# Optimization experiments

Hardware: AMD Instinct MI355X
Metric: run time of the kernel (lower is better)

The kernel has to match this reference:

```python
import jax, jax.numpy as jnp
import numpy as np

EPS = 1e-12  # guard sqrt at zero


def setup_inputs() -> dict:
    key = jax.random.key(0)
    k1, k2, k3 = jax.random.split(key, 3)
    B, N = 16, 2048
    pred_points = jax.random.normal(k1, (B, N, 3), dtype=jnp.float32)
    target_points = jax.random.normal(k2, (B, N, 3), dtype=jnp.float32)
    # binary symmetry flag per object, kept float for the blend
    sym_flag = (jax.random.uniform(k3, (B,)) > 0.5).astype(jnp.float32)
    return {"pred_points": pred_points, "target_points": target_points, "sym_flag": sym_flag}


def reference(pred_points, target_points, sym_flag):
    # Chamfer (ADD-S style): per pred point, min Euclidean distance to any target point.
    # Pairwise squared distances via ||p||^2 + ||t||^2 - 2 p.t  -> [B, N, M]
    p2 = jnp.sum(pred_points * pred_points, axis=-1)[:, :, None]   # [B,N,1]
    t2 = jnp.sum(target_points * target_points, axis=-1)[:, None, :]  # [B,1,M]
    cross = jnp.einsum('bnd,bmd->bnm', pred_points, target_points)  # [B,N,M]
    d2 = p2 + t2 - 2.0 * cross
    dist = jnp.sqrt(jnp.maximum(d2, EPS))                           # [B,N,M]
    sym_dis = jnp.min(dist, axis=2).mean(axis=1)                    # [B]

    # L2 (ADD style): per-point correspondence distance.
    asym_dis = jnp.linalg.norm(pred_points - target_points, axis=2).mean(axis=1)  # [B]

    all_loss = sym_flag * sym_dis + (1.0 - sym_flag) * asym_dis
    return all_loss.mean()
```

## Files before the change

kernel.cpp:

```cpp
#include <hip/hip_runtime.h>
#include <hip/hip_bf16.h>
#include <math.h>


typedef short short8 __attribute__((ext_vector_type(8)));
typedef float f32x16 __attribute__((ext_vector_type(16)));

__device__ __forceinline__ unsigned short f2bf(float f) {
  unsigned u = __float_as_uint(f);
  u = u + 0x7FFFu + ((u >> 16) & 1u);
  return (unsigned short)(u >> 16);
}
__device__ __forceinline__ float bf2f(unsigned short h) {
  return __uint_as_float(((unsigned)h) << 16);
}

#define K1_TPB 256
#define TQS 512
#define PPANEL 256

__global__ __launch_bounds__(K1_TPB) void chamfer_mfma_kernel(
    const float* __restrict__ pred, const float* __restrict__ targ,
    float* __restrict__ minS, float* __restrict__ out, int N, int B) {
  __shared__ short8 sA[2][TQS];

  const int blk = blockIdx.x;
  const int tq = blk & 3;
  const int pp = (blk >> 2) & 7;
  const int b = blk >> 5;

  if (blk == 0 && threadIdx.x == 0) out[0] = 0.f;

  const float* tb = targ + ((size_t)b * N + tq * TQS) * 3;
  for (int t = threadIdx.x; t < TQS; t += K1_TPB) {
    const float x = tb[t * 3], y = tb[t * 3 + 1], z = tb[t * 3 + 2];
    const unsigned short thx = f2bf(x), thy = f2bf(y), thz = f2bf(z);
    const unsigned short tlx = f2bf(x - bf2f(thx));
    const unsigned short tly = f2bf(y - bf2f(thy));
    const unsigned short tlz = f2bf(z - bf2f(thz));
    const float q = 0.5f * (x * x + y * y + z * z);
    const unsigned short qh = f2bf(q), ql = f2bf(q - bf2f(qh));
    sA[0][t] = short8{(short)thx, (short)thy, (short)thz, (short)thx,
                      (short)thy, (short)thz, (short)tlx, (short)tly};
    sA[1][t] = short8{(short)tlz, (short)qh, (short)ql, 0, 0, 0, 0, 0};
  }

  const int lane = threadIdx.x & 63;
  const int w = threadIdx.x >> 6;
  const int g = lane >> 5;
  const int l31 = lane & 31;
  const int colBase = pp * PPANEL + w * 64;

  short8 bf0, bf1;
  {
#pragma unroll
    for (int pt = 0; pt < 2; ++pt) {
      const int c = colBase + pt * 32 + l31;
      const float* pq = pred + ((size_t)b * N + c) * 3;
      const float x = pq[0], y = pq[1], z = pq[2];
      const unsigned short hx = f2bf(-x), hy = f2bf(-y), hz = f2bf(-z);
      const unsigned short lx = f2bf(-x - bf2f(hx));
      const unsigned short ly = f2bf(-y - bf2f(hy));
      const unsigned short lz = f2bf(-z - bf2f(hz));
      short8 r;
      if (g == 0)
        r = short8{(short)hx, (short)hy, (short)hz, (short)lx,
                   (short)ly, (short)lz, (short)hx, (short)hy};
      else
        r = short8{(short)hz, (short)0x3F80, (short)0x3F80, 0, 0, 0, 0, 0};
      if (pt == 0) bf0 = r; else bf1 = r;
    }
  }
  __syncthreads();

  const f32x16 zc = {0.f, 0.f, 0.f, 0.f, 0.f, 0.f, 0.f, 0.f,
                     0.f, 0.f, 0.f, 0.f, 0.f, 0.f, 0.f, 0.f};
  float rm0[8], rm1[8];
#pragma unroll
  for (int i = 0; i < 8; ++i) { rm0[i] = 3.4e38f; rm1[i] = 3.4e38f; }

#pragma unroll 4
  for (int ta = 0; ta < TQS / 32; ++ta) {
    const short8 a = sA[g][ta * 32 + l31];
    const f32x16 d0 = __builtin_amdgcn_mfma_f32_32x32x16_bf16(a, bf0, zc, 0, 0, 0);
    const f32x16 d1 = __builtin_amdgcn_mfma_f32_32x32x16_bf16(a, bf1, zc, 0, 0, 0);
#pragma unroll
    for (int i = 0; i < 8; ++i) {
      rm0[i] = fminf(rm0[i], fminf(d0[2 * i], d0[2 * i + 1]));
      rm1[i] = fminf(rm1[i], fminf(d1[2 * i], d1[2 * i + 1]));
    }
  }

  float m0 = rm0[0], m1 = rm1[0];
#pragma unroll
  for (int i = 1; i < 8; ++i) { m0 = fminf(m0, rm0[i]); m1 = fminf(m1, rm1[i]); }
  m0 = fminf(m0, __shfl_xor(m0, 32));
  m1 = fminf(m1, __shfl_xor(m1, 32));

  if (lane < 32) {
    float* dst = minS + ((size_t)(b * 4 + tq)) * N;
    dst[colBase + lane] = m0;
    dst[colBase + 32 + lane] = m1;
  }
}

__global__ __launch_bounds__(256) void chamfer_final_kernel(
    const float* __restrict__ pred, const float* __restrict__ targ,
    const float* __restrict__ minS, const float* __restrict__ sym_flag,
    float* __restrict__ out, int N, int B, float invNB) {
  const int blk = blockIdx.x;
  const int b = blk >> 3;
  const int i = (blk & 7) * 256 + threadIdx.x;
  const size_t col = (size_t)b * N + i;

  float m = minS[(size_t)(b * 4 + 0) * N + i];
  m = fminf(m, minS[(size_t)(b * 4 + 1) * N + i]);
  m = fminf(m, minS[(size_t)(b * 4 + 2) * N + i]);
  m = fminf(m, minS[(size_t)(b * 4 + 3) * N + i]);

  const float px = pred[col * 3], py = pred[col * 3 + 1], pz = pred[col * 3 + 2];
  const float tx = targ[col * 3], ty = targ[col * 3 + 1], tz = targ[col * 3 + 2];
  const float hp2 = 0.5f * (px * px + py * py + pz * pz);
  const float dsym = sqrtf(fmaxf(2.f * (m + hp2), 1e-12f));
  const float dx = px - tx, dy = py - ty, dz = pz - tz;
  const float dasym = sqrtf(dx * dx + dy * dy + dz * dz);
  const float f = sym_flag[b];

  float c = (f * dsym + (1.f - f) * dasym) * invNB;
#pragma unroll
  for (int off = 32; off > 0; off >>= 1) c += __shfl_xor(c, off);
  __shared__ float sW[4];
  if ((threadIdx.x & 63) == 0) sW[threadIdx.x >> 6] = c;
  __syncthreads();
  if (threadIdx.x == 0) atomicAdd(out, sW[0] + sW[1] + sW[2] + sW[3]);
}

extern "C" void kernel_launch(void* const* d_in, const int* in_sizes, int n_in,
                              void* d_out, int out_size, void* d_ws, size_t ws_size,
                              hipStream_t stream) {
  const float* pred = (const float*)d_in[0];
  const float* targ = (const float*)d_in[1];
  const float* sym_flag = (const float*)d_in[2];
  float* out = (float*)d_out;

  const int B = in_sizes[2];
  const int N = in_sizes[0] / (B * 3);

  float* minS = (float*)d_ws;

  const int grid1 = B * 4 * (N / PPANEL);
  chamfer_mfma_kernel<<<grid1, K1_TPB, 0, stream>>>(pred, targ, minS, out, N, B);

  const int grid2 = B * (N / 256);
  chamfer_final_kernel<<<grid2, 256, 0, stream>>>(
      pred, targ, minS, sym_flag, out, N, B, 1.0f / (float)(N * B));
}
```

Baseline: 15.94 us.

## Fuse min-reduction and loss into MFMA kernel with full target set per block

Each block now loads the entire 2048-point target set for its batch into shared memory and processes 128 pred columns, so it computes the full nearest-neighbour minimum without splitting targets across blocks. The per-point sym/asym loss is then computed in the same kernel and written as per-wave partials. A single-block kernel sums them deterministically, replacing the global-memory min buffer, the second per-point pass and the atomic. The trade-off is that every block re-packs all 2048 targets into 64 KB of LDS, which cuts occupancy, and each wave issues one MFMA per step where it used to issue two.

```diff
diff --git a/kernel.cpp b/kernel.cpp
--- a/kernel.cpp
+++ b/kernel.cpp
@@ -15,24 +15,21 @@
   return __uint_as_float(((unsigned)h) << 16);
 }
 
-#define K1_TPB 256
-#define TQS 512
-#define PPANEL 256
+#define TPB 256
+#define NPTS 2048
 
-__global__ __launch_bounds__(K1_TPB) void chamfer_mfma_kernel(
+__global__ __launch_bounds__(TPB) void chamfer_fused_mfma_kernel(
     const float* __restrict__ pred, const float* __restrict__ targ,
-    float* __restrict__ minS, float* __restrict__ out, int N, int B) {
-  __shared__ short8 sA[2][TQS];
+    const float* __restrict__ sym_flag, float* __restrict__ partial,
+    int N, int B, int panelsPerBatch) {
+  __shared__ short8 sA[2][NPTS];
 
   const int blk = blockIdx.x;
-  const int tq = blk & 3;
-  const int pp = (blk >> 2) & 7;
-  const int b = blk >> 5;
+  const int pp = blk % panelsPerBatch;
+  const int b = blk / panelsPerBatch;
 
-  if (blk == 0 && threadIdx.x == 0) out[0] = 0.f;
-
-  const float* tb = targ + ((size_t)b * N + tq * TQS) * 3;
-  for (int t = threadIdx.x; t < TQS; t += K1_TPB) {
+  const float* tb = targ + (size_t)b * N * 3;
+  for (int t = threadIdx.x; t < N; t += TPB) {
     const float x = tb[t * 3], y = tb[t * 3 + 1], z = tb[t * 3 + 2];
     const unsigned short thx = f2bf(x), thy = f2bf(y), thz = f2bf(z);
     const unsigned short tlx = f2bf(x - bf2f(thx));
@@ -49,90 +46,68 @@
   const int w = threadIdx.x >> 6;
   const int g = lane >> 5;
   const int l31 = lane & 31;
-  const int colBase = pp * PPANEL + w * 64;
+  const int col = pp * 128 + w * 32 + l31;
 
-  short8 bf0, bf1;
+  const float* pq = pred + ((size_t)b * N + col) * 3;
+  const float px = pq[0], py = pq[1], pz = pq[2];
+  short8 bfr;
   {
-#pragma unroll
-    for (int pt = 0; pt < 2; ++pt) {
-      const int c = colBase + pt * 32 + l31;
-      const float* pq = pred + ((size_t)b * N + c) * 3;
-      const float x = pq[0], y = pq[1], z = pq[2];
-      const unsigned short hx = f2bf(-x), hy = f2bf(-y), hz = f2bf(-z);
-      const unsigned short lx = f2bf(-x - bf2f(hx));
-      const unsigned short ly = f2bf(-y - bf2f(hy));
-      const unsigned short lz = f2bf(-z - bf2f(hz));
-      short8 r;
-      if (g == 0)
-        r = short8{(short)hx, (short)hy, (short)hz, (short)lx,
+    const unsigned short hx = f2bf(-px), hy = f2bf(-py), hz = f2bf(-pz);
+    const unsigned short lx = f2bf(-px - bf2f(hx));
+    const unsigned short ly = f2bf(-py - bf2f(hy));
+    const unsigned short lz = f2bf(-pz - bf2f(hz));
+    if (g == 0)
+      bfr = short8{(short)hx, (short)hy, (short)hz, (short)lx,
                    (short)ly, (short)lz, (short)hx, (short)hy};
-      else
-        r = short8{(short)hz, (short)0x3F80, (short)0x3F80, 0, 0, 0, 0, 0};
-      if (pt == 0) bf0 = r; else bf1 = r;
-    }
+    else
+      bfr = short8{(short)hz, (short)0x3F80, (short)0x3F80, 0, 0, 0, 0, 0};
   }
   __syncthreads();
 
   const f32x16 zc = {0.f, 0.f, 0.f, 0.f, 0.f, 0.f, 0.f, 0.f,
                      0.f, 0.f, 0.f, 0.f, 0.f, 0.f, 0.f, 0.f};
-  float rm0[8], rm1[8];
+  float rm[8];
 #pragma unroll
-  for (int i = 0; i < 8; ++i) { rm0[i] = 3.4e38f; rm1[i] = 3.4e38f; }
+  for (int i = 0; i < 8; ++i) rm[i] = 3.4e38f;
 
 #pragma unroll 4
-  for (int ta = 0; ta < TQS / 32; ++ta) {
+  for (int ta = 0; ta < NPTS / 32; ++ta) {
     const short8 a = sA[g][ta * 32 + l31];
-    const f32x16 d0 = __builtin_amdgcn_mfma_f32_32x32x16_bf16(a, bf0, zc, 0, 0, 0);
-    const f32x16 d1 = __builtin_amdgcn_mfma_f32_32x32x16_bf16(a, bf1, zc, 0, 0, 0);
+    const f32x16 d = __builtin_amdgcn_mfma_f32_32x32x16_bf16(a, bfr, zc, 0, 0, 0);
 #pragma unroll
-    for (int i = 0; i < 8; ++i) {
-      rm0[i] = fminf(rm0[i], fminf(d0[2 * i], d0[2 * i + 1]));
-      rm1[i] = fminf(rm1[i], fminf(d1[2 * i], d1[2 * i + 1]));
-    }
+    for (int i = 0; i < 8; ++i)
+      rm[i] = fminf(rm[i], fminf(d[2 * i], d[2 * i + 1]));
   }
 
-  float m0 = rm0[0], m1 = rm1[0];
+  float m = rm[0];
 #pragma unroll
-  for (int i = 1; i < 8; ++i) { m0 = fminf(m0, rm0[i]); m1 = fminf(m1, rm1[i]); }
-  m0 = fminf(m0, __shfl_xor(m0, 32));
-  m1 = fminf(m1, __shfl_xor(m1, 32));
+  for (int i = 1; i < 8; ++i) m = fminf(m, rm[i]);
+  m = fminf(m, __shfl_xor(m, 32));
 
-  if (lane < 32) {
-    float* dst = minS + ((size_t)(b * 4 + tq)) * N;
-    dst[colBase + lane] = m0;
-    dst[colBase + 32 + lane] = m1;
-  }
+  const float hp2 = 0.5f * (px * px + py * py + pz * pz);
+  const float dsym = sqrtf(fmaxf(2.f * (m + hp2), 1e-12f));
+  const float* tq = targ + ((size_t)b * N + col) * 3;
+  const float dx = px - tq[0], dy = py - tq[1], dz = pz - tq[2];
+  const float dasym = sqrtf(dx * dx + dy * dy + dz * dz);
+  const float f = sym_flag[b];
+  float c = (lane < 32) ? (f * dsym + (1.f - f) * dasym) : 0.f;
+#pragma unroll
+  for (int off = 32; off > 0; off >>= 1) c += __shfl_xor(c, off);
+  if (lane == 0) partial[blk * 4 + w] = c;
 }
 
-__global__ __launch_bounds__(256) void chamfer_final_kernel(
-    const float* __restrict__ pred, const float* __restrict__ targ,
-    const float* __restrict__ minS, const float* __restrict__ sym_flag,
-    float* __restrict__ out, int N, int B, float invNB) {
-  const int blk = blockIdx.x;
-  const int b = blk >> 3;
-  const int i = (blk & 7) * 256 + threadIdx.x;
-  const size_t col = (size_t)b * N + i;
-
-  float m = minS[(size_t)(b * 4 + 0) * N + i];
-  m = fminf(m, minS[(size_t)(b * 4 + 1) * N + i]);
-  m = fminf(m, minS[(size_t)(b * 4 + 2) * N + i]);
-  m = fminf(m, minS[(size_t)(b * 4 + 3) * N + i]);
-
-  const float px = pred[col * 3], py = pred[col * 3 + 1], pz = pred[col * 3 + 2];
-  const float tx = targ[col * 3], ty = targ[col * 3 + 1], tz = targ[col * 3 + 2];
-  const float hp2 = 0.5f * (px * px + py * py + pz * pz);
-  const float dsym = sqrtf(fmaxf(2.f * (m + hp2), 1e-12f));
-  const float dx = px - tx, dy = py - ty, dz = pz - tz;
-  const float dasym = sqrtf(dx * dx + dy * dy + dz * dz);
-  const float f = sym_flag[b];
-
-  float c = (f * dsym + (1.f - f) * dasym) * invNB;
+__global__ __launch_bounds__(256) void chamfer_sum_kernel(
+    const float* __restrict__ partial, float* __restrict__ out,
+    int nPartial, float invNB) {
+  const float4 v = ((const float4*)partial)[threadIdx.x];
+  float s = (v.x + v.y) + (v.z + v.w);
 #pragma unroll
-  for (int off = 32; off > 0; off >>= 1) c += __shfl_xor(c, off);
+  for (int off = 32; off > 0; off >>= 1) s += __shfl_xor(s, off);
   __shared__ float sW[4];
-  if ((threadIdx.x & 63) == 0) sW[threadIdx.x >> 6] = c;
+  if ((threadIdx.x & 63) == 0) sW[threadIdx.x >> 6] = s;
   __syncthreads();
-  if (threadIdx.x == 0) atomicAdd(out, sW[0] + sW[1] + sW[2] + sW[3]);
+  if (threadIdx.x == 0)
+    out[0] = (sW[0] + sW[1] + sW[2] + sW[3]) * invNB;
 }
 
 extern "C" void kernel_launch(void* const* d_in, const int* in_sizes, int n_in,
@@ -146,12 +121,13 @@
   const int B = in_sizes[2];
   const int N = in_sizes[0] / (B * 3);
 
-  float* minS = (float*)d_ws;
+  const int panelsPerBatch = N / 128;
+  const int grid1 = B * panelsPerBatch;
+  float* partial = (float*)d_ws;
 
-  const int grid1 = B * 4 * (N / PPANEL);
-  chamfer_mfma_kernel<<<grid1, K1_TPB, 0, stream>>>(pred, targ, minS, out, N, B);
+  chamfer_fused_mfma_kernel<<<grid1, TPB, 0, stream>>>(
+      pred, targ, sym_flag, partial, N, B, panelsPerBatch);
 
-  const int grid2 = B * (N / 256);
-  chamfer_final_kernel<<<grid2, 256, 0, stream>>>(
-      pred, targ, minS, sym_flag, out, N, B, 1.0f / (float)(N * B));
+  chamfer_sum_kernel<<<1, 256, 0, stream>>>(
+      partial, out, grid1 * 4, 1.0f / (float)(N * B));
 }
```

New measurement: 16.94 us. 1.06x slower.

## Precompute bf16 split operands in a separate pack kernel before MFMA pass

Applied to the files above, without the earlier changes.

Adds a pack kernel that converts target and pred points once into hi/lo bf16 short8 operand layouts in workspace, instead of each MFMA block redoing the conversion from strided fp32 loads. The MFMA kernel then loads the prepacked vectors directly into shared memory and registers, and gets launch_bounds min-blocks hint of 2. This removes redundant conversion work (targets were converted 8x, once per pred panel) at the cost of an extra kernel launch and a workspace round trip.

```diff
diff --git a/kernel.cpp b/kernel.cpp
--- a/kernel.cpp
+++ b/kernel.cpp
@@ -15,13 +15,51 @@
   return __uint_as_float(((unsigned)h) << 16);
 }
 
-#define K1_TPB 256
 #define TQS 512
 #define PPANEL 256
 
-__global__ __launch_bounds__(K1_TPB) void chamfer_mfma_kernel(
+__global__ __launch_bounds__(256) void chamfer_pack_kernel(
     const float* __restrict__ pred, const float* __restrict__ targ,
-    float* __restrict__ minS, float* __restrict__ out, int N, int B) {
+    short8* __restrict__ pA, short8* __restrict__ pB,
+    float* __restrict__ out, int N, int B) {
+  const int idx = blockIdx.x * 256 + threadIdx.x;
+  if (idx == 0) out[0] = 0.f;
+  if (idx >= B * N) return;
+  const int b = idx / N, t = idx % N;
+
+  {
+    const float x = targ[(size_t)idx * 3], y = targ[(size_t)idx * 3 + 1],
+                z = targ[(size_t)idx * 3 + 2];
+    const unsigned short thx = f2bf(x), thy = f2bf(y), thz = f2bf(z);
+    const unsigned short tlx = f2bf(x - bf2f(thx));
+    const unsigned short tly = f2bf(y - bf2f(thy));
+    const unsigned short tlz = f2bf(z - bf2f(thz));
+    const float q = 0.5f * (x * x + y * y + z * z);
+    const unsigned short qh = f2bf(q), ql = f2bf(q - bf2f(qh));
+    pA[(size_t)(b * 2 + 0) * N + t] =
+        short8{(short)thx, (short)thy, (short)thz, (short)thx,
+               (short)thy, (short)thz, (short)tlx, (short)tly};
+    pA[(size_t)(b * 2 + 1) * N + t] =
+        short8{(short)tlz, (short)qh, (short)ql, 0, 0, 0, 0, 0};
+  }
+  {
+    const float x = pred[(size_t)idx * 3], y = pred[(size_t)idx * 3 + 1],
+                z = pred[(size_t)idx * 3 + 2];
+    const unsigned short hx = f2bf(-x), hy = f2bf(-y), hz = f2bf(-z);
+    const unsigned short lx = f2bf(-x - bf2f(hx));
+    const unsigned short ly = f2bf(-y - bf2f(hy));
+    const unsigned short lz = f2bf(-z - bf2f(hz));
+    pB[(size_t)(b * 2 + 0) * N + t] =
+        short8{(short)hx, (short)hy, (short)hz, (short)lx,
+               (short)ly, (short)lz, (short)hx, (short)hy};
+    pB[(size_t)(b * 2 + 1) * N + t] =
+        short8{(short)hz, (short)0x3F80, (short)0x3F80, 0, 0, 0, 0, 0};
+  }
+}
+
+__global__ __launch_bounds__(256, 2) void chamfer_mfma_kernel(
+    const short8* __restrict__ pA, const short8* __restrict__ pB,
+    float* __restrict__ minS, int N, int B) {
   __shared__ short8 sA[2][TQS];
 
   const int blk = blockIdx.x;
@@ -29,20 +67,11 @@
   const int pp = (blk >> 2) & 7;
   const int b = blk >> 5;
 
-  if (blk == 0 && threadIdx.x == 0) out[0] = 0.f;
-
-  const float* tb = targ + ((size_t)b * N + tq * TQS) * 3;
-  for (int t = threadIdx.x; t < TQS; t += K1_TPB) {
-    const float x = tb[t * 3], y = tb[t * 3 + 1], z = tb[t * 3 + 2];
-    const unsigned short thx = f2bf(x), thy = f2bf(y), thz = f2bf(z);
-    const unsigned short tlx = f2bf(x - bf2f(thx));
-    const unsigned short tly = f2bf(y - bf2f(thy));
-    const unsigned short tlz = f2bf(z - bf2f(thz));
-    const float q = 0.5f * (x * x + y * y + z * z);
-    const unsigned short qh = f2bf(q), ql = f2bf(q - bf2f(qh));
-    sA[0][t] = short8{(short)thx, (short)thy, (short)thz, (short)thx,
-                      (short)thy, (short)thz, (short)tlx, (short)tly};
-    sA[1][t] = short8{(short)tlz, (short)qh, (short)ql, 0, 0, 0, 0, 0};
+  const short8* g0 = pA + ((size_t)(b * 2 + 0) * N + tq * TQS);
+  const short8* g1 = pA + ((size_t)(b * 2 + 1) * N + tq * TQS);
+  for (int i = threadIdx.x; i < TQS; i += 256) {
+    sA[0][i] = g0[i];
+    sA[1][i] = g1[i];
   }
 
   const int lane = threadIdx.x & 63;
@@ -51,26 +80,9 @@
   const int l31 = lane & 31;
   const int colBase = pp * PPANEL + w * 64;
 
-  short8 bf0, bf1;
-  {
-#pragma unroll
-    for (int pt = 0; pt < 2; ++pt) {
-      const int c = colBase + pt * 32 + l31;
-      const float* pq = pred + ((size_t)b * N + c) * 3;
-      const float x = pq[0], y = pq[1], z = pq[2];
-      const unsigned short hx = f2bf(-x), hy = f2bf(-y), hz = f2bf(-z);
-      const unsigned short lx = f2bf(-x - bf2f(hx));
-      const unsigned short ly = f2bf(-y - bf2f(hy));
-      const unsigned short lz = f2bf(-z - bf2f(hz));
-      short8 r;
-      if (g == 0)
-        r = short8{(short)hx, (short)hy, (short)hz, (short)lx,
-                   (short)ly, (short)lz, (short)hx, (short)hy};
-      else
-        r = short8{(short)hz, (short)0x3F80, (short)0x3F80, 0, 0, 0, 0, 0};
-      if (pt == 0) bf0 = r; else bf1 = r;
-    }
-  }
+  const short8* pb = pB + ((size_t)(b * 2 + g) * N + colBase);
+  const short8 bf0 = pb[l31];
+  const short8 bf1 = pb[32 + l31];
   __syncthreads();
 
   const f32x16 zc = {0.f, 0.f, 0.f, 0.f, 0.f, 0.f, 0.f, 0.f,
@@ -146,10 +158,15 @@
   const int B = in_sizes[2];
   const int N = in_sizes[0] / (B * 3);
 
-  float* minS = (float*)d_ws;
+  short8* pA = (short8*)d_ws;
+  short8* pB = pA + (size_t)B * 2 * N;
+  float* minS = (float*)(pB + (size_t)B * 2 * N);
+
+  const int gridPack = (B * N + 255) / 256;
+  chamfer_pack_kernel<<<gridPack, 256, 0, stream>>>(pred, targ, pA, pB, out, N, B);
 
   const int grid1 = B * 4 * (N / PPANEL);
-  chamfer_mfma_kernel<<<grid1, K1_TPB, 0, stream>>>(pred, targ, minS, out, N, B);
+  chamfer_mfma_kernel<<<grid1, 256, 0, stream>>>(pA, pB, minS, N, B);
 
   const int grid2 = B * (N / 256);
   chamfer_final_kernel<<<grid2, 256, 0, stream>>>(
```

Result: slower. 20.93 us (+31.3%).

## Fuse min-reduction and loss epilogue into MFMA kernel, split targets across waves

Applied to the files above, without the earlier changes.

Each block now owns 64 pred columns and all 2048 targets. The four waves each scan a quarter of the targets and combine their minima through shared memory. The block then computes the sym/asym loss in place and writes one partial sum per block, and a single-block kernel adds these up, replacing the atomic. This removes the minS round trip through global memory and the second full-width pass. In exchange, every block converts all 2048 targets into LDS (64 KB), which is four times more redundant target preprocessing and lowers occupancy.

```diff
diff --git a/kernel.cpp b/kernel.cpp
--- a/kernel.cpp
+++ b/kernel.cpp
@@ -15,24 +15,22 @@
   return __uint_as_float(((unsigned)h) << 16);
 }
 
-#define K1_TPB 256
-#define TQS 512
-#define PPANEL 256
+#define TPB 256
+#define NPTS 2048
 
-__global__ __launch_bounds__(K1_TPB) void chamfer_mfma_kernel(
+__global__ __launch_bounds__(TPB, 2) void chamfer_main_kernel(
     const float* __restrict__ pred, const float* __restrict__ targ,
-    float* __restrict__ minS, float* __restrict__ out, int N, int B) {
-  __shared__ short8 sA[2][TQS];
+    const float* __restrict__ sym_flag, float* __restrict__ partial,
+    int N, int B, int panelsPerBatch) {
+  __shared__ short8 sA[2][NPTS];
+  __shared__ float sm[4][64];
 
   const int blk = blockIdx.x;
-  const int tq = blk & 3;
-  const int pp = (blk >> 2) & 7;
-  const int b = blk >> 5;
+  const int pp = blk % panelsPerBatch;
+  const int b = blk / panelsPerBatch;
 
-  if (blk == 0 && threadIdx.x == 0) out[0] = 0.f;
-
-  const float* tb = targ + ((size_t)b * N + tq * TQS) * 3;
-  for (int t = threadIdx.x; t < TQS; t += K1_TPB) {
+  const float* tb = targ + (size_t)b * N * 3;
+  for (int t = threadIdx.x; t < NPTS; t += TPB) {
     const float x = tb[t * 3], y = tb[t * 3 + 1], z = tb[t * 3 + 2];
     const unsigned short thx = f2bf(x), thy = f2bf(y), thz = f2bf(z);
     const unsigned short tlx = f2bf(x - bf2f(thx));
@@ -49,27 +47,25 @@
   const int w = threadIdx.x >> 6;
   const int g = lane >> 5;
   const int l31 = lane & 31;
-  const int colBase = pp * PPANEL + w * 64;
+  const int colBase = pp * 64;
 
   short8 bf0, bf1;
-  {
 #pragma unroll
-    for (int pt = 0; pt < 2; ++pt) {
-      const int c = colBase + pt * 32 + l31;
-      const float* pq = pred + ((size_t)b * N + c) * 3;
-      const float x = pq[0], y = pq[1], z = pq[2];
-      const unsigned short hx = f2bf(-x), hy = f2bf(-y), hz = f2bf(-z);
-      const unsigned short lx = f2bf(-x - bf2f(hx));
-      const unsigned short ly = f2bf(-y - bf2f(hy));
-      const unsigned short lz = f2bf(-z - bf2f(hz));
-      short8 r;
-      if (g == 0)
-        r = short8{(short)hx, (short)hy, (short)hz, (short)lx,
-                   (short)ly, (short)lz, (short)hx, (short)hy};
-      else
-        r = short8{(short)hz, (short)0x3F80, (short)0x3F80, 0, 0, 0, 0, 0};
-      if (pt == 0) bf0 = r; else bf1 = r;
-    }
+  for (int pt = 0; pt < 2; ++pt) {
+    const int col = colBase + pt * 32 + l31;
+    const float* pq = pred + ((size_t)b * N + col) * 3;
+    const float x = pq[0], y = pq[1], z = pq[2];
+    const unsigned short hx = f2bf(-x), hy = f2bf(-y), hz = f2bf(-z);
+    const unsigned short lx = f2bf(-x - bf2f(hx));
+    const unsigned short ly = f2bf(-y - bf2f(hy));
+    const unsigned short lz = f2bf(-z - bf2f(hz));
+    short8 r;
+    if (g == 0)
+      r = short8{(short)hx, (short)hy, (short)hz, (short)lx,
+                 (short)ly, (short)lz, (short)hx, (short)hy};
+    else
+      r = short8{(short)hz, (short)0x3F80, (short)0x3F80, 0, 0, 0, 0, 0};
+    if (pt == 0) bf0 = r; else bf1 = r;
   }
   __syncthreads();
 
@@ -80,8 +76,8 @@
   for (int i = 0; i < 8; ++i) { rm0[i] = 3.4e38f; rm1[i] = 3.4e38f; }
 
 #pragma unroll 4
-  for (int ta = 0; ta < TQS / 32; ++ta) {
-    const short8 a = sA[g][ta * 32 + l31];
+  for (int ta = 0; ta < 16; ++ta) {
+    const short8 a = sA[g][w * 512 + ta * 32 + l31];
     const f32x16 d0 = __builtin_amdgcn_mfma_f32_32x32x16_bf16(a, bf0, zc, 0, 0, 0);
     const f32x16 d1 = __builtin_amdgcn_mfma_f32_32x32x16_bf16(a, bf1, zc, 0, 0, 0);
 #pragma unroll
@@ -96,43 +92,40 @@
   for (int i = 1; i < 8; ++i) { m0 = fminf(m0, rm0[i]); m1 = fminf(m1, rm1[i]); }
   m0 = fminf(m0, __shfl_xor(m0, 32));
   m1 = fminf(m1, __shfl_xor(m1, 32));
+  if (lane < 32) {
+    sm[w][l31] = m0;
+    sm[w][32 + l31] = m1;
+  }
+  __syncthreads();
 
-  if (lane < 32) {
-    float* dst = minS + ((size_t)(b * 4 + tq)) * N;
-    dst[colBase + lane] = m0;
-    dst[colBase + 32 + lane] = m1;
+  if (threadIdx.x < 64) {
+    const int i = threadIdx.x;
+    const float mm = fminf(fminf(sm[0][i], sm[1][i]), fminf(sm[2][i], sm[3][i]));
+    const size_t gc = (size_t)b * N + colBase + i;
+    const float x = pred[gc * 3], y = pred[gc * 3 + 1], z = pred[gc * 3 + 2];
+    const float tx = targ[gc * 3], ty = targ[gc * 3 + 1], tz = targ[gc * 3 + 2];
+    const float hp2 = 0.5f * (x * x + y * y + z * z);
+    const float dsym = sqrtf(fmaxf(2.f * (mm + hp2), 1e-12f));
+    const float dx = x - tx, dy = y - ty, dz = z - tz;
+    const float dasym = sqrtf(dx * dx + dy * dy + dz * dz);
+    const float f = sym_flag[b];
+    float c = f * dsym + (1.f - f) * dasym;
+#pragma unroll
+    for (int off = 32; off > 0; off >>= 1) c += __shfl_xor(c, off);
+    if (i == 0) partial[blk] = c;
   }
 }
 
-__global__ __launch_bounds__(256) void chamfer_final_kernel(
-    const float* __restrict__ pred, const float* __restrict__ targ,
-    const float* __restrict__ minS, const float* __restrict__ sym_flag,
-    float* __restrict__ out, int N, int B, float invNB) {
-  const int blk = blockIdx.x;
-  const int b = blk >> 3;
-  const int i = (blk & 7) * 256 + threadIdx.x;
-  const size_t col = (size_t)b * N + i;
-
-  float m = minS[(size_t)(b * 4 + 0) * N + i];
-  m = fminf(m, minS[(size_t)(b * 4 + 1) * N + i]);
-  m = fminf(m, minS[(size_t)(b * 4 + 2) * N + i]);
-  m = fminf(m, minS[(size_t)(b * 4 + 3) * N + i]);
-
-  const float px = pred[col * 3], py = pred[col * 3 + 1], pz = pred[col * 3 + 2];
-  const float tx = targ[col * 3], ty = targ[col * 3 + 1], tz = targ[col * 3 + 2];
-  const float hp2 = 0.5f * (px * px + py * py + pz * pz);
-  const float dsym = sqrtf(fmaxf(2.f * (m + hp2), 1e-12f));
-  const float dx = px - tx, dy = py - ty, dz = pz - tz;
-  const float dasym = sqrtf(dx * dx + dy * dy + dz * dz);
-  const float f = sym_flag[b];
-
-  float c = (f * dsym + (1.f - f) * dasym) * invNB;
+__global__ __launch_bounds__(256) void chamfer_sum_kernel(
+    const float* __restrict__ partial, float* __restrict__ out, float invNB) {
+  const int t = threadIdx.x;
+  float s = partial[t] + partial[t + 256];
 #pragma unroll
-  for (int off = 32; off > 0; off >>= 1) c += __shfl_xor(c, off);
+  for (int off = 32; off > 0; off >>= 1) s += __shfl_xor(s, off);
   __shared__ float sW[4];
-  if ((threadIdx.x & 63) == 0) sW[threadIdx.x >> 6] = c;
+  if ((t & 63) == 0) sW[t >> 6] = s;
   __syncthreads();
-  if (threadIdx.x == 0) atomicAdd(out, sW[0] + sW[1] + sW[2] + sW[3]);
+  if (t == 0) out[0] = (sW[0] + sW[1] + sW[2] + sW[3]) * invNB;
 }
 
 extern "C" void kernel_launch(void* const* d_in, const int* in_sizes, int n_in,
@@ -146,12 +139,12 @@
   const int B = in_sizes[2];
   const int N = in_sizes[0] / (B * 3);
 
-  float* minS = (float*)d_ws;
+  const int panelsPerBatch = N / 64;
+  const int grid = B * panelsPerBatch;
+  float* partial = (float*)d_ws;
 
-  const int grid1 = B * 4 * (N / PPANEL);
-  chamfer_mfma_kernel<<<grid1, K1_TPB, 0, stream>>>(pred, targ, minS, out, N, B);
-
-  const int grid2 = B * (N / 256);
-  chamfer_final_kernel<<<grid2, 256, 0, stream>>>(
-      pred, targ, minS, sym_flag, out, N, B, 1.0f / (float)(N * B));
+  chamfer_main_kernel<<<grid, TPB, 0, stream>>>(pred, targ, sym_flag, partial,
+                                                N, B, panelsPerBatch);
+  chamfer_sum_kernel<<<1, 256, 0, stream>>>(partial, out,
+                                            1.0f / (float)(N * B));
 }
```

Result: faster. 14.86 us (-6.8%).
